# Kernel optimization log

Measured on AMD Instinct MI355X. Metric: run time of the kernel, lower is better.

Reference implementation:

```python
import jax, jax.numpy as jnp
import numpy as np

B, N, M, D = 2, 8192, 8192, 2
CIN, COUT, E, K = 32, 32, 16, 32
GAMMA = float(E * E)  # RBF sharpness
MUS = jnp.linspace(0.0, 1.0, E)  # RBF centers on [0, 1] (points drawn from unit square)


def setup_inputs() -> dict:
    key = jax.random.key(0)
    k1, k2, k3, k4, k5 = jax.random.split(key, 5)
    points_in = jax.random.uniform(k1, (B, N, D), dtype=jnp.float32)
    values_in = jax.random.normal(k2, (B, N, CIN), dtype=jnp.float32)
    points_out = jax.random.uniform(k3, (B, M, D), dtype=jnp.float32)
    coeff = jax.random.normal(k4, (CIN, COUT, E), dtype=jnp.float32)
    bias = jax.random.normal(k5, (COUT,), dtype=jnp.float32)
    return {"points_in": points_in, "values_in": values_in, "points_out": points_out,
            "coeff": coeff, "bias": bias}


def reference(points_in, values_in, points_out, coeff, bias):
    # u_inverse_v = g(points_out)^{-1} applied to points_in; for the translation
    # group this is the pairwise relative position tensor. Torch computes it
    # under no_grad -> stop_gradient here.
    uiv = points_out[:, :, None, :] - points_in[:, None, :, :]        # [B, M, N, D]
    norms = jnp.linalg.norm(uiv, axis=-1)                              # [B, M, N]
    neg_r, idx = jax.lax.top_k(-norms, K)                              # smallest K dists
    r_k = jax.lax.stop_gradient(-neg_r)                                # [B, M, K]
    idx = jax.lax.stop_gradient(idx)                                   # [B, M, K] int32
    uiv_k = jax.lax.stop_gradient(
        jnp.take_along_axis(uiv, idx[..., None], axis=2))              # [B, M, K, D]
    # det == 1 for translation group (non-Tensor in torch -> branch skipped)
    # gather neighbor values: values_in broadcast over M, gathered along N
    vals_k = jnp.take_along_axis(values_in[:, None, :, :], idx[..., None], axis=2)  # [B, M, K, CIN]
    # Gaussian radial kernel basis evaluated on |u_inverse_v|
    kernel_b = jnp.exp(-GAMMA * (r_k[..., None] - MUS) ** 2)           # [B, M, K, E]
    out = jnp.einsum('ioe,bmke,bmki->bmo', coeff, kernel_b, vals_k) / K
    out = out + bias
    return uiv_k, idx, out
```

## Files before the change

kernel.cpp:

```cpp
#include <hip/hip_runtime.h>
#include <cstdint>
#include <cstddef>

constexpr int BB   = 2;
constexpr int NN   = 8192;
constexpr int MM   = 8192;
constexpr int CIN  = 32;
constexpr int COUT = 32;
constexpr int EE   = 16;
constexpr int KK   = 32;
constexpr int GRID = 32;
constexpr int NCELL = GRID * GRID;

#define QPB2 8
#define CAP 128
#define VROW 36
#define VQS  1156
#define ECH 4
#define CLBASE 580

#define R0_FAST 0.0432f

constexpr size_t OFS_COEFFT = 0;
constexpr size_t OFS_COUNTS = 65536;
constexpr size_t OFS_CURSOR = 73728;
constexpr size_t OFS_STARTS = 81920;
constexpr size_t OFS_PTSS   = 90624;
constexpr size_t OFS_IDXS   = 221696;

__global__ __launch_bounds__(256) void prep_coeff_zero(const float* __restrict__ coeff,
                                                       float* __restrict__ coeff2,
                                                       int* __restrict__ cz) {
    int tid = blockIdx.x * 256 + threadIdx.x;
    if (tid < 2 * 2 * NCELL) cz[tid] = 0;
    if (tid >= EE * CIN * COUT) return;
    int o = tid & 31;
    int i = (tid >> 5) & 31;
    int e = tid >> 10;
    coeff2[tid] = coeff[(i * COUT + o) * EE + e];
}

__device__ __forceinline__ int cell_of(float2 p) {
    int cx = min(GRID - 1, max(0, (int)(p.x * (float)GRID)));
    int cy = min(GRID - 1, max(0, (int)(p.y * (float)GRID)));
    return cy * GRID + cx;
}

__global__ __launch_bounds__(256) void bin_count(const float* __restrict__ pts,
                                                 int* __restrict__ counts) {
    int t = blockIdx.x * 256 + threadIdx.x;
    int b = t >> 13, i = t & (NN - 1);
    float2 p = ((const float2*)pts)[(size_t)b * NN + i];
    atomicAdd(&counts[b * NCELL + cell_of(p)], 1);
}

__global__ __launch_bounds__(1024) void bin_scan(const int* __restrict__ counts,
                                                 int* __restrict__ starts) {
    __shared__ int wsum[16];
    const int b    = blockIdx.x;
    const int t    = threadIdx.x;
    const int lane = t & 63, wv = t >> 6;
    int s = counts[b * NCELL + t];
#pragma unroll
    for (int off = 1; off < 64; off <<= 1) {
        const int v = __shfl_up(s, off, 64);
        if (lane >= off) s += v;
    }
    if (lane == 63) wsum[wv] = s;
    __syncthreads();
    if (wv == 0) {
        int ws = (lane < 16) ? wsum[lane] : 0;
#pragma unroll
        for (int off = 1; off < 16; off <<= 1) {
            const int v = __shfl_up(ws, off, 64);
            if (lane >= off) ws += v;
        }
        if (lane < 16) wsum[lane] = ws;
    }
    __syncthreads();
    const int woff = (wv > 0) ? wsum[wv - 1] : 0;
    starts[b * (NCELL + 1) + t + 1] = s + woff;
    if (t == 0) starts[b * (NCELL + 1)] = 0;
}

__global__ __launch_bounds__(256) void bin_scatter(const float* __restrict__ pts,
                                                   const int* __restrict__ starts,
                                                   int* __restrict__ cursor,
                                                   float2* __restrict__ pts_s,
                                                   int* __restrict__ idx_s) {
    int t = blockIdx.x * 256 + threadIdx.x;
    int b = t >> 13, i = t & (NN - 1);
    float2 p = ((const float2*)pts)[(size_t)b * NN + i];
    int cell = cell_of(p);
    int pos = starts[b * (NCELL + 1) + cell] + atomicAdd(&cursor[b * NCELL + cell], 1);
    pts_s[(size_t)b * NN + pos] = p;
    idx_s[(size_t)b * NN + pos] = i;
}

__global__ __launch_bounds__(256) void conv_fused(
    const float2* __restrict__ pts_s, const int* __restrict__ idx_s,
    const int* __restrict__ starts,
    const float* __restrict__ points_in, const float* __restrict__ values_in,
    const float* __restrict__ points_out,
    const float* __restrict__ coeff2, const float* __restrict__ bias,
    float* __restrict__ out_uiv, float* __restrict__ out_idx,
    float* __restrict__ out_val)
{
    __shared__ alignas(16) float POOL[QPB2 * VQS];

    const int tid   = threadIdx.x;
    const int sl    = tid & 31;
    const int qslot = tid >> 5;
    const int half  = qslot & 1;
    const int wid   = blockIdx.x * QPB2 + qslot;
    const int b     = wid >> 13;
    const int m     = wid & (MM - 1);

    unsigned long long* KEYq = (unsigned long long*)&POOL[qslot * VQS];
    float* VLq = &POOL[qslot * VQS];

    const float2* PS = pts_s + (size_t)b * NN;
    const int*    IS = idx_s + (size_t)b * NN;
    const int*    ST = starts + b * (NCELL + 1);
    const float2* P  = ((const float2*)points_in) + (size_t)b * NN;
    const float2  q  = ((const float2*)points_out)[(size_t)b * MM + m];

    const float INF = __builtin_inff();
    const float h = 1.0f / (float)GRID;
    const unsigned lmlt32 = (1u << sl) - 1u;

    float bd;
    int   bi;
    bool  ok = false;

    {
        float tau = R0_FAST;
        {
            const float bx = fminf(q.x, 1.0f - q.x);
            const float by = fminf(q.y, 1.0f - q.y);
#pragma unroll
            for (int it = 0; it < 3; ++it) {
                const float wx = 0.5f + 0.5f * fminf(bx / tau, 1.0f);
                const float wy = 0.5f + 0.5f * fminf(by / tau, 1.0f);
                tau = R0_FAST * __frsqrt_rn(wx * wy);
            }
        }
        const float tau2  = tau * tau;
        const float tau2a = tau2 * (1.0f + 2e-6f);

        const int xlo = (int)fmaxf((q.x - tau) * (float)GRID, 0.0f);
        const int xhi = (int)fminf((q.x + tau) * (float)GRID, (float)(GRID - 1));
        const int ylo = (int)fmaxf((q.y - tau) * (float)GRID, 0.0f);
        const int yhi = (int)fminf((q.y + tau) * (float)GRID, (float)(GRID - 1));
        const int nrows = yhi - ylo + 1;

        int sv = 0, ev = 0;
        if (sl < nrows) {
            sv = ST[(ylo + sl) * GRID + xlo];
            ev = ST[(ylo + sl) * GRID + xhi + 1];
        }

        int base = 0, nin = 0;
        for (int r = 0; r < nrows; ++r) {
            const int s = __shfl(sv, r, 32), e = __shfl(ev, r, 32);
            for (int j0 = s; j0 < e; j0 += 32) {
                const int j = j0 + sl;
                const bool valid = (j < e);
                float2 p = make_float2(2.0f, 2.0f);
                if (valid) p = PS[j];
                const float dx = q.x - p.x, dy = q.y - p.y;
                const float d2 = __builtin_fmaf(dy, dy, __fmul_rn(dx, dx));
                const bool adm = valid && (d2 <= tau2a);
                const unsigned bmA = (unsigned)(__ballot(adm) >> (half << 5));
                const unsigned bmS = (unsigned)(__ballot(valid && (d2 <= tau2)) >> (half << 5));
                nin += __popc(bmS);
                if (bmA) {
                    const float ex = __fsqrt_rn(__fadd_rn(__fmul_rn(dx, dx),
                                                          __fmul_rn(dy, dy)));
                    const int pos = base + __popc(bmA & lmlt32);
                    if (adm && pos < CAP)
                        KEYq[pos] =
                            ((unsigned long long)__float_as_uint(ex) << 32) | (unsigned)IS[j];
                    base += __popc(bmA);
                }
            }
        }

        ok = (nin >= 32) && (base <= CAP);
        if (ok) {
            unsigned long long k0 = (sl      < base) ? KEYq[sl]      : ~0ull;
            unsigned long long k1 = (sl + 32 < base) ? KEYq[sl + 32] : ~0ull;
            int r0 = 0, r1 = 0;
            if (!__any(base > 64)) {
                for (int t = 0; t < base; ++t) {
                    const unsigned long long kt = KEYq[t];
                    r0 += (kt < k0) ? 1 : 0;
                    r1 += (kt < k1) ? 1 : 0;
                }
            } else {
                unsigned long long k2 = (sl + 64 < base) ? KEYq[sl + 64] : ~0ull;
                unsigned long long k3 = (sl + 96 < base) ? KEYq[sl + 96] : ~0ull;
                int r2 = 0, r3 = 0;
                for (int t = 0; t < base; ++t) {
                    const unsigned long long kt = KEYq[t];
                    r0 += (kt < k0) ? 1 : 0;
                    r1 += (kt < k1) ? 1 : 0;
                    r2 += (kt < k2) ? 1 : 0;
                    r3 += (kt < k3) ? 1 : 0;
                }
                if (sl + 64 < base && r2 < 32) KEYq[r2] = k2;
                if (sl + 96 < base && r3 < 32) KEYq[r3] = k3;
            }
            if (sl      < base && r0 < 32) KEYq[r0] = k0;
            if (sl + 32 < base && r1 < 32) KEYq[r1] = k1;
            const unsigned long long kf = KEYq[sl];
            bd = __uint_as_float((unsigned)(kf >> 32));
            bi = (int)(unsigned)(kf & 0xffffffffull);

            const float tau32 = __shfl(bd, 31, 32);
            float g = INF;
            if (xlo > 0)        g = fminf(g, q.x - (float)xlo * h);
            if (xhi < GRID - 1) g = fminf(g, (float)(xhi + 1) * h - q.x);
            if (ylo > 0)        g = fminf(g, q.y - (float)ylo * h);
            if (yhi < GRID - 1) g = fminf(g, (float)(yhi + 1) * h - q.y);
            ok = (tau32 < g * (1.0f - 4e-6f));
        }
    }

    if (!ok) {
        const int cx = min(GRID - 1, max(0, (int)(q.x * (float)GRID)));
        const int cy = min(GRID - 1, max(0, (int)(q.y * (float)GRID)));
        int L = 2;
        for (;;) {
            const int xlo = max(cx - L, 0), xhi = min(cx + L, GRID - 1);
            const int ylo = max(cy - L, 0), yhi = min(cy + L, GRID - 1);
            const int nrows = yhi - ylo + 1;

            int sv = 0, ev = 0;
            if (sl < nrows) {
                sv = ST[(ylo + sl) * GRID + xlo];
                ev = ST[(ylo + sl) * GRID + xhi + 1];
            }

            float mn1 = INF, mn2 = INF;
            for (int r = 0; r < nrows; ++r) {
                const int s = __shfl(sv, r, 32), e = __shfl(ev, r, 32);
                for (int j = s + sl; j < e; j += 32) {
                    const float2 p = PS[j];
                    const float dx = q.x - p.x, dy = q.y - p.y;
                    const float d2 = __builtin_fmaf(dy, dy, __fmul_rn(dx, dx));
                    const float big = fmaxf(mn1, d2);
                    mn1 = fminf(mn1, d2);
                    mn2 = fminf(mn2, big);
                }
            }

            {
                float v = mn2;
#pragma unroll
                for (int k = 2; k <= 32; k <<= 1) {
#pragma unroll
                    for (int j = k >> 1; j > 0; j >>= 1) {
                        const float o = __shfl_xor(v, j, 32);
                        const bool up = ((sl & k) == 0), lower = ((sl & j) == 0);
                        const float mnv = fminf(v, o), mxv = fmaxf(v, o);
                        v = (lower == up) ? mnv : mxv;
                    }
                }
                mn2 = __shfl(v, 15, 32);
            }
            const float tau2b = mn2 * (1.0f + 4e-6f);

            int base = 0;
            for (int r = 0; r < nrows; ++r) {
                const int s = __shfl(sv, r, 32), e = __shfl(ev, r, 32);
                for (int j0 = s; j0 < e; j0 += 32) {
                    const int j = j0 + sl;
                    const bool valid = (j < e);
                    float2 p = make_float2(0.f, 0.f);
                    if (valid) p = PS[j];
                    const float dx = q.x - p.x, dy = q.y - p.y;
                    const float d2 = __builtin_fmaf(dy, dy, __fmul_rn(dx, dx));
                    const bool pred = valid && (d2 <= tau2b);
                    const unsigned bm = (unsigned)(__ballot(pred) >> (half << 5));
                    if (bm) {
                        const float ex = __fsqrt_rn(__fadd_rn(__fmul_rn(dx, dx),
                                                              __fmul_rn(dy, dy)));
                        const int pos = base + __popc(bm & lmlt32);
                        if (pred && pos < CAP)
                            KEYq[pos] =
                                ((unsigned long long)__float_as_uint(ex) << 32) | (unsigned)IS[j];
                        base += __popc(bm);
                    }
                }
            }

            if (base <= CAP) {
                unsigned long long k0 = (sl      < base) ? KEYq[sl]      : ~0ull;
                unsigned long long k1 = (sl + 32 < base) ? KEYq[sl + 32] : ~0ull;
                int r0 = 0, r1 = 0;
                if (!__any(base > 64)) {
                    for (int t = 0; t < base; ++t) {
                        const unsigned long long kt = KEYq[t];
                        r0 += (kt < k0) ? 1 : 0;
                        r1 += (kt < k1) ? 1 : 0;
                    }
                } else {
                    unsigned long long k2 = (sl + 64 < base) ? KEYq[sl + 64] : ~0ull;
                    unsigned long long k3 = (sl + 96 < base) ? KEYq[sl + 96] : ~0ull;
                    int r2 = 0, r3 = 0;
                    for (int t = 0; t < base; ++t) {
                        const unsigned long long kt = KEYq[t];
                        r0 += (kt < k0) ? 1 : 0;
                        r1 += (kt < k1) ? 1 : 0;
                        r2 += (kt < k2) ? 1 : 0;
                        r3 += (kt < k3) ? 1 : 0;
                    }
                    if (sl + 64 < base && r2 < 32) KEYq[r2] = k2;
                    if (sl + 96 < base && r3 < 32) KEYq[r3] = k3;
                }
                if (sl      < base && r0 < 32) KEYq[r0] = k0;
                if (sl + 32 < base && r1 < 32) KEYq[r1] = k1;
                if (base < 32 && sl >= base) KEYq[sl] = ~0ull;
                const unsigned long long kf = KEYq[sl];
                bd = __uint_as_float((unsigned)(kf >> 32));
                bi = (int)(unsigned)(kf & 0xffffffffull);
            } else {
                float fd = INF; int fi = 0x7FFFFFFF;
                for (int r = 0; r < nrows; ++r) {
                    const int s = __shfl(sv, r, 32), e = __shfl(ev, r, 32);
                    for (int j0 = s; j0 < e; j0 += 32) {
                        const int j = j0 + sl;
                        const bool valid = (j < e);
                        float2 p = make_float2(0.f, 0.f);
                        int vi0 = 0x7FFFFFFF;
                        if (valid) { p = PS[j]; vi0 = IS[j]; }
                        const float dx = q.x - p.x, dy = q.y - p.y;
                        const float d2 = __builtin_fmaf(dy, dy, __fmul_rn(dx, dx));
                        unsigned cm = (unsigned)(__ballot(valid && (d2 <= tau2b)) >> (half << 5));
                        const float ex = __fsqrt_rn(__fadd_rn(__fmul_rn(dx, dx),
                                                              __fmul_rn(dy, dy)));
                        while (cm) {
                            const int l = __builtin_ctz(cm); cm &= cm - 1;
                            const float v  = __shfl(ex, l, 32);
                            const int   vi = __shfl(vi0, l, 32);
                            const bool cl = (fd < v) || (fd == v && fi < vi);
                            const int pos = __popc((unsigned)(__ballot(cl) >> (half << 5)));
                            const float sd = __shfl_up(fd, 1, 32);
                            const int   si = __shfl_up(fi, 1, 32);
                            fd = (sl < pos) ? fd : ((sl == pos) ? v  : sd);
                            fi = (sl < pos) ? fi : ((sl == pos) ? vi : si);
                        }
                    }
                }
                bd = fd; bi = fi;
            }

            const float tau = __shfl(bd, 31, 32);
            float g = INF;
            if (xlo > 0)        g = fminf(g, q.x - (float)xlo * h);
            if (xhi < GRID - 1) g = fminf(g, (float)(xhi + 1) * h - q.x);
            if (ylo > 0)        g = fminf(g, q.y - (float)ylo * h);
            if (yhi < GRID - 1) g = fminf(g, (float)(yhi + 1) * h - q.y);
            if (tau < g * (1.0f - 4e-6f)) break;
            L += 2;
            if (L > GRID - 1) L = GRID - 1;
        }
    }

    {
        const float2 pk = P[bi];
        float2 u;
        u.x = q.x - pk.x;
        u.y = q.y - pk.y;
        ((float2*)out_uiv)[(size_t)wid * KK + sl] = u;
        out_idx[(size_t)wid * KK + sl] = (float)bi;
    }

    {
        const float4* src = (const float4*)(values_in + ((size_t)b * NN + bi) * CIN);
        const float4 r0 = src[0], r1 = src[1], r2 = src[2], r3 = src[3];
        const float4 r4 = src[4], r5 = src[5], r6 = src[6], r7 = src[7];
        float4* dst = (float4*)(VLq + sl * VROW);
        dst[0] = r0; dst[1] = r1; dst[2] = r2; dst[3] = r3;
        dst[4] = r4; dst[5] = r5; dst[6] = r6; dst[7] = r7;
    }

    {
        const int e2 = sl >> 2;
        const int iq = sl & 3;
        const float mu0 = (float)(2 * e2)     * (1.0f / 15.0f);
        const float mu1 = (float)(2 * e2 + 1) * (1.0f / 15.0f);
        float4 A0a = make_float4(0.f, 0.f, 0.f, 0.f);
        float4 A0b = A0a, A1a = A0a, A1b = A0a;
#pragma unroll 8
        for (int k = 0; k < KK; ++k) {
            const float rk = __shfl(bd, k, 32);
            const float d0 = rk - mu0;
            const float d1 = rk - mu1;
            const float w0 = __expf(-256.0f * d0 * d0);
            const float w1 = __expf(-256.0f * d1 * d1);
            const float4* vr = (const float4*)(VLq + k * VROW + iq * 8);
            const float4 va = vr[0], vb = vr[1];
            A0a.x += w0 * va.x; A0a.y += w0 * va.y; A0a.z += w0 * va.z; A0a.w += w0 * va.w;
            A0b.x += w0 * vb.x; A0b.y += w0 * vb.y; A0b.z += w0 * vb.z; A0b.w += w0 * vb.w;
            A1a.x += w1 * va.x; A1a.y += w1 * va.y; A1a.z += w1 * va.z; A1a.w += w1 * va.w;
            A1b.x += w1 * vb.x; A1b.y += w1 * vb.y; A1b.z += w1 * vb.z; A1b.w += w1 * vb.w;
        }
        float4* t0 = (float4*)(VLq + (2 * e2)     * VROW + iq * 8);
        float4* t1 = (float4*)(VLq + (2 * e2 + 1) * VROW + iq * 8);
        t0[0] = A0a; t0[1] = A0b;
        t1[0] = A1a; t1[1] = A1b;
    }

    {
        const int w  = tid >> 6;
        const int rq = (tid >> 3) & 7;
        const int ro = tid & 7;
        float4 s4 = make_float4(0.f, 0.f, 0.f, 0.f);
        const float* Tq = &POOL[rq * VQS];
#pragma unroll
        for (int ec = 0; ec < EE / ECH; ++ec) {
            __syncthreads();
            {
                const float4* src = (const float4*)(coeff2 + ec * (ECH * CIN * COUT));
#pragma unroll
                for (int j = 0; j < 4; ++j) {
                    const int idx = tid + j * 256;
                    const int ch  = idx >> 7;
                    const int o4  = idx & 127;
                    ((float4*)(&POOL[ch * VQS + CLBASE]))[o4] = src[idx];
                }
            }
            __syncthreads();
#pragma unroll
            for (int el = 0; el < ECH; ++el) {
                const int e = ec * ECH + el;
                const float* Trow = Tq + e * VROW + 8 * w;
                const float4 ta = *(const float4*)(Trow);
                const float4 tb = *(const float4*)(Trow + 4);
                const float* Crow = &POOL[(el * 2 + (w >> 1)) * VQS + CLBASE
                                          + (w & 1) * 256 + ro * 4];
#pragma unroll
                for (int ir = 0; ir < 4; ++ir) {
                    const float t = (ir == 0) ? ta.x : (ir == 1) ? ta.y
                                  : (ir == 2) ? ta.z : ta.w;
                    const float4 c = *(const float4*)(Crow + ir * COUT);
                    s4.x += t * c.x; s4.y += t * c.y;
                    s4.z += t * c.z; s4.w += t * c.w;
                }
#pragma unroll
                for (int ir = 0; ir < 4; ++ir) {
                    const float t = (ir == 0) ? tb.x : (ir == 1) ? tb.y
                                  : (ir == 2) ? tb.z : tb.w;
                    const float4 c = *(const float4*)(Crow + (4 + ir) * COUT);
                    s4.x += t * c.x; s4.y += t * c.y;
                    s4.z += t * c.z; s4.w += t * c.w;
                }
            }
        }
        __syncthreads();
        float4* PART = (float4*)POOL;
        PART[tid] = s4;
        __syncthreads();
        if (w == 0) {
            const float4 p0 = PART[tid];
            const float4 p1 = PART[tid + 64];
            const float4 p2 = PART[tid + 128];
            const float4 p3 = PART[tid + 192];
            const float4 bv = *(const float4*)(bias + ro * 4);
            float4 ov;
            ov.x = (p0.x + p1.x + p2.x + p3.x) * (1.0f / 32.0f) + bv.x;
            ov.y = (p0.y + p1.y + p2.y + p3.y) * (1.0f / 32.0f) + bv.y;
            ov.z = (p0.z + p1.z + p2.z + p3.z) * (1.0f / 32.0f) + bv.z;
            ov.w = (p0.w + p1.w + p2.w + p3.w) * (1.0f / 32.0f) + bv.w;
            const int qw = blockIdx.x * QPB2 + rq;
            *(float4*)(out_val + (size_t)qw * COUT + ro * 4) = ov;
        }
    }
}

extern "C" void kernel_launch(void* const* d_in, const int* in_sizes, int n_in,
                              void* d_out, int out_size, void* d_ws, size_t ws_size,
                              hipStream_t stream) {
    const float* points_in  = (const float*)d_in[0];
    const float* values_in  = (const float*)d_in[1];
    const float* points_out = (const float*)d_in[2];
    const float* coeff      = (const float*)d_in[3];
    const float* bias       = (const float*)d_in[4];

    float* out     = (float*)d_out;
    float* out_uiv = out;
    float* out_idx = out + (size_t)BB * MM * KK * 2;
    float* out_val = out_idx + (size_t)BB * MM * KK;

    char* ws = (char*)d_ws;
    float*  coeff2 = (float*)(ws + OFS_COEFFT);
    int*    counts = (int*)  (ws + OFS_COUNTS);
    int*    cursor = (int*)  (ws + OFS_CURSOR);
    int*    strts  = (int*)  (ws + OFS_STARTS);
    float2* pts_s  = (float2*)(ws + OFS_PTSS);
    int*    idx_s  = (int*)  (ws + OFS_IDXS);

    hipLaunchKernelGGL(prep_coeff_zero, dim3(64), dim3(256), 0, stream,
                       coeff, coeff2, counts);
    hipLaunchKernelGGL(bin_count, dim3(64), dim3(256), 0, stream, points_in, counts);
    hipLaunchKernelGGL(bin_scan, dim3(BB), dim3(1024), 0, stream, counts, strts);
    hipLaunchKernelGGL(bin_scatter, dim3(64), dim3(256), 0, stream,
                       points_in, strts, cursor, pts_s, idx_s);

    const int blocks = (BB * MM) / QPB2;
    hipLaunchKernelGGL(conv_fused, dim3(blocks), dim3(256), 0, stream,
                       pts_s, idx_s, strts, points_in, values_in, points_out,
                       coeff2, bias, out_uiv, out_idx, out_val);
}
```

Measured before the change: 60.38 us.

## Shrink per-query LDS stripe with XOR-swizzled value rows and smaller coeff chunks

Changes the shared-memory layout of the fused conv kernel. Gathered neighbour value rows are now stored unpadded (32 floats) with an XOR swizzle on float4 slots to avoid bank conflicts, and the per-query stripe shrinks from 1156 to 1024 floats. The basis-weighted tile gets a padded row stride and a per-query offset, and coefficient staging moves from four-E to two-E chunks laid out differently. Total LDS per block drops, which could raise occupancy, but the coefficient loop now has twice as many barrier-separated stages.

```diff
diff --git a/kernel.cpp b/kernel.cpp
--- a/kernel.cpp
+++ b/kernel.cpp
@@ -14,10 +14,11 @@
 
 #define QPB2 8
 #define CAP 128
-#define VROW 36
-#define VQS  1156
-#define ECH 4
-#define CLBASE 580
+#define VROW 32
+#define TROW 36
+#define STRIPE 1024
+#define ECH 2
+#define CLBASE 604
 
 #define R0_FAST 0.0432f
 
@@ -106,7 +107,7 @@
     float* __restrict__ out_uiv, float* __restrict__ out_idx,
     float* __restrict__ out_val)
 {
-    __shared__ alignas(16) float POOL[QPB2 * VQS];
+    __shared__ alignas(16) float POOL[QPB2 * STRIPE];
 
     const int tid   = threadIdx.x;
     const int sl    = tid & 31;
@@ -116,8 +117,9 @@
     const int b     = wid >> 13;
     const int m     = wid & (MM - 1);
 
-    unsigned long long* KEYq = (unsigned long long*)&POOL[qslot * VQS];
-    float* VLq = &POOL[qslot * VQS];
+    unsigned long long* KEYq = (unsigned long long*)&POOL[qslot * STRIPE];
+    float* VLq = &POOL[qslot * STRIPE];
+    float* TLq = VLq + qslot * 4;
 
     const float2* PS = pts_s + (size_t)b * NN;
     const int*    IS = idx_s + (size_t)b * NN;
@@ -382,8 +384,9 @@
         const float4 r0 = src[0], r1 = src[1], r2 = src[2], r3 = src[3];
         const float4 r4 = src[4], r5 = src[5], r6 = src[6], r7 = src[7];
         float4* dst = (float4*)(VLq + sl * VROW);
-        dst[0] = r0; dst[1] = r1; dst[2] = r2; dst[3] = r3;
-        dst[4] = r4; dst[5] = r5; dst[6] = r6; dst[7] = r7;
+        const int sw = sl & 7;
+        dst[0 ^ sw] = r0; dst[1 ^ sw] = r1; dst[2 ^ sw] = r2; dst[3 ^ sw] = r3;
+        dst[4 ^ sw] = r4; dst[5 ^ sw] = r5; dst[6 ^ sw] = r6; dst[7 ^ sw] = r7;
     }
 
     {
@@ -400,15 +403,17 @@
             const float d1 = rk - mu1;
             const float w0 = __expf(-256.0f * d0 * d0);
             const float w1 = __expf(-256.0f * d1 * d1);
-            const float4* vr = (const float4*)(VLq + k * VROW + iq * 8);
-            const float4 va = vr[0], vb = vr[1];
+            const float4* vrow = (const float4*)(VLq + k * VROW);
+            const int kw = k & 7;
+            const float4 va = vrow[(iq * 2)     ^ kw];
+            const float4 vb = vrow[(iq * 2 + 1) ^ kw];
             A0a.x += w0 * va.x; A0a.y += w0 * va.y; A0a.z += w0 * va.z; A0a.w += w0 * va.w;
             A0b.x += w0 * vb.x; A0b.y += w0 * vb.y; A0b.z += w0 * vb.z; A0b.w += w0 * vb.w;
             A1a.x += w1 * va.x; A1a.y += w1 * va.y; A1a.z += w1 * va.z; A1a.w += w1 * va.w;
             A1b.x += w1 * vb.x; A1b.y += w1 * vb.y; A1b.z += w1 * vb.z; A1b.w += w1 * vb.w;
         }
-        float4* t0 = (float4*)(VLq + (2 * e2)     * VROW + iq * 8);
-        float4* t1 = (float4*)(VLq + (2 * e2 + 1) * VROW + iq * 8);
+        float4* t0 = (float4*)(TLq + (2 * e2)     * TROW + iq * 8);
+        float4* t1 = (float4*)(TLq + (2 * e2 + 1) * TROW + iq * 8);
         t0[0] = A0a; t0[1] = A0b;
         t1[0] = A1a; t1[1] = A1b;
     }
@@ -418,29 +423,28 @@
         const int rq = (tid >> 3) & 7;
         const int ro = tid & 7;
         float4 s4 = make_float4(0.f, 0.f, 0.f, 0.f);
-        const float* Tq = &POOL[rq * VQS];
+        const float* Tq = &POOL[rq * STRIPE] + rq * 4;
 #pragma unroll
         for (int ec = 0; ec < EE / ECH; ++ec) {
             __syncthreads();
             {
                 const float4* src = (const float4*)(coeff2 + ec * (ECH * CIN * COUT));
 #pragma unroll
-                for (int j = 0; j < 4; ++j) {
+                for (int j = 0; j < 2; ++j) {
                     const int idx = tid + j * 256;
-                    const int ch  = idx >> 7;
-                    const int o4  = idx & 127;
-                    ((float4*)(&POOL[ch * VQS + CLBASE]))[o4] = src[idx];
+                    const int ch  = idx >> 6;
+                    const int o4  = idx & 63;
+                    ((float4*)(&POOL[ch * STRIPE + CLBASE]))[o4] = src[idx];
                 }
             }
             __syncthreads();
 #pragma unroll
             for (int el = 0; el < ECH; ++el) {
                 const int e = ec * ECH + el;
-                const float* Trow = Tq + e * VROW + 8 * w;
+                const float* Trow = Tq + e * TROW + 8 * w;
                 const float4 ta = *(const float4*)(Trow);
                 const float4 tb = *(const float4*)(Trow + 4);
-                const float* Crow = &POOL[(el * 2 + (w >> 1)) * VQS + CLBASE
-                                          + (w & 1) * 256 + ro * 4];
+                const float* Crow = &POOL[(el * 4 + w) * STRIPE + CLBASE + ro * 4];
 #pragma unroll
                 for (int ir = 0; ir < 4; ++ir) {
                     const float t = (ir == 0) ? ta.x : (ir == 1) ? ta.y
```

Result: slower. 63.26 us (+4.8%).
